# Kernel tuning notes

Measured on AMD Instinct MI355X. Metric: run time of the kernel, lower is better.

## Reference

```python
import jax, jax.numpy as jnp
import numpy as np

N = 20000      # nodes
E = 320000     # edges
F = 32         # node_feat_dim
H = 128        # hidden_dim
HEADS = 4
DH = 128       # out_channels per head (PyG TransformerConv semantics)
L = 2          # number of GNNBlocks actually built


def _ln(x, s, b, eps=1e-5):
    m = x.mean(-1, keepdims=True)
    v = ((x - m) ** 2).mean(-1, keepdims=True)
    return (x - m) / jnp.sqrt(v + eps) * s + b


def setup_inputs() -> dict:
    key = jax.random.key(0)
    ks = jax.random.split(key, 16)
    nrm = lambda k, sh, sc=0.05: jax.random.normal(k, sh, dtype=jnp.float32) * sc
    inp = {}
    inp['x'] = jax.random.normal(ks[0], (N, F), dtype=jnp.float32)
    inp['edge_index'] = jax.random.randint(ks[1], (2, E), 0, N)
    inp['Win'] = nrm(ks[2], (F, H))
    inp['b_in'] = jnp.zeros((H,), jnp.float32)
    inp['ln1_s'] = jnp.ones((L, H), jnp.float32)
    inp['ln1_b'] = jnp.zeros((L, H), jnp.float32)
    inp['Wq'] = nrm(ks[3], (L, H, HEADS * DH))
    inp['bq'] = jnp.zeros((L, HEADS * DH), jnp.float32)
    inp['Wk'] = nrm(ks[4], (L, H, HEADS * DH))
    inp['bk'] = jnp.zeros((L, HEADS * DH), jnp.float32)
    inp['Wv'] = nrm(ks[5], (L, H, HEADS * DH))
    inp['bv'] = jnp.zeros((L, HEADS * DH), jnp.float32)
    inp['Wskip'] = nrm(ks[6], (L, H, H))
    inp['bskip'] = jnp.zeros((L, H), jnp.float32)
    inp['Wbeta'] = nrm(ks[7], (L, 3 * H, 1))
    inp['ln2_s'] = jnp.ones((L, H), jnp.float32)
    inp['ln2_b'] = jnp.zeros((L, H), jnp.float32)
    inp['W1'] = nrm(ks[8], (L, H, 4 * H))
    inp['b1'] = jnp.zeros((L, 4 * H), jnp.float32)
    inp['W2'] = nrm(ks[9], (L, 4 * H, H))
    inp['b2'] = jnp.zeros((L, H), jnp.float32)
    inp['g1'] = jnp.ones((L,), jnp.float32)
    inp['g2'] = jnp.ones((L,), jnp.float32)
    inp['lno_s'] = jnp.ones((H,), jnp.float32)
    inp['lno_b'] = jnp.zeros((H,), jnp.float32)
    return inp


def reference(x, edge_index, Win, b_in, ln1_s, ln1_b, Wq, bq, Wk, bk, Wv, bv,
              Wskip, bskip, Wbeta, ln2_s, ln2_b, W1, b1, W2, b2, g1, g2,
              lno_s, lno_b):
    src, dst = edge_index[0], edge_index[1]  # messages flow src -> dst
    n = x.shape[0]
    scale = 1.0 / np.sqrt(DH).astype(np.float32)
    h = x @ Win + b_in  # [N,H]
    for l in range(L):
        # --- pre-norm TransformerConv (heads=4, concat=False, beta=True) ---
        hn = _ln(h, ln1_s[l], ln1_b[l])
        q = (hn @ Wq[l] + bq[l]).reshape(n, HEADS, DH)
        k = (hn @ Wk[l] + bk[l]).reshape(n, HEADS, DH)
        v = (hn @ Wv[l] + bv[l]).reshape(n, HEADS, DH)
        # per-edge attention logits [E, HEADS]
        alpha = jnp.einsum('ehd,ehd->eh', q[dst], k[src]) * scale
        # segment softmax over incoming edges of each target node
        amax = jax.ops.segment_max(alpha, dst, num_segments=n)  # [N,HEADS]
        num = jnp.exp(alpha - amax[dst])
        den = jax.ops.segment_sum(num, dst, num_segments=n)      # [N,HEADS]
        a = num / den[dst]                                       # [E,HEADS]
        # scatter-aggregate weighted values, then mean over heads (concat=False)
        agg = jax.ops.segment_sum(a[:, :, None] * v[src], dst, num_segments=n)
        out = agg.mean(axis=1)                                   # [N,H]
        # root skip + beta gate
        xr = hn @ Wskip[l] + bskip[l]
        beta = jax.nn.sigmoid(
            jnp.concatenate([out, xr, out - xr], axis=-1) @ Wbeta[l])  # [N,1]
        attn = beta * xr + (1.0 - beta) * out
        h = h + g1[l] * attn
        # --- pre-norm FFN ---
        hn2 = _ln(h, ln2_s[l], ln2_b[l])
        ffn = jax.nn.gelu(hn2 @ W1[l] + b1[l], approximate=False) @ W2[l] + b2[l]
        h = h + g2[l] * ffn
    return _ln(h, lno_s, lno_b)
```

## Files before the change

kernel.cpp:

```cpp
#include <hip/hip_runtime.h>
#include <hip/hip_bf16.h>
#include <math.h>

#define NN 20000
#define NE 320000

typedef unsigned short ushort_t;
typedef unsigned short ushortx8 __attribute__((ext_vector_type(8)));
typedef short s16x8 __attribute__((ext_vector_type(8)));
typedef float f32x4 __attribute__((ext_vector_type(4)));
typedef float f32x2 __attribute__((ext_vector_type(2)));

__device__ __forceinline__ float us2f(unsigned short u){
  return __uint_as_float(((unsigned)u) << 16);
}
__device__ __forceinline__ unsigned short f2us(float f){
  unsigned u = __float_as_uint(f);
  unsigned r = (u + 0x7fffu + ((u >> 16) & 1u)) >> 16;
  return (unsigned short)r;
}
__device__ __forceinline__ void e4m3x8_to_f32(uint2 d, float* out){
  f32x2 a = __builtin_amdgcn_cvt_pk_f32_fp8(d.x, false);
  f32x2 b = __builtin_amdgcn_cvt_pk_f32_fp8(d.x, true);
  f32x2 c = __builtin_amdgcn_cvt_pk_f32_fp8(d.y, false);
  f32x2 e = __builtin_amdgcn_cvt_pk_f32_fp8(d.y, true);
  out[0] = a.x; out[1] = a.y; out[2] = b.x; out[3] = b.y;
  out[4] = c.x; out[5] = c.y; out[6] = e.x; out[7] = e.y;
}
__device__ __forceinline__ uint2 f32x8_to_e4m3(const float* f){
  unsigned lo = __builtin_amdgcn_cvt_pk_fp8_f32(f[0], f[1], 0u, false);
  lo = __builtin_amdgcn_cvt_pk_fp8_f32(f[2], f[3], lo, true);
  unsigned hi = __builtin_amdgcn_cvt_pk_fp8_f32(f[4], f[5], 0u, false);
  hi = __builtin_amdgcn_cvt_pk_fp8_f32(f[6], f[7], hi, true);
  return make_uint2(lo, hi);
}
template<int CTRL>
__device__ __forceinline__ float dpp_add(float x){
  int t = __builtin_amdgcn_update_dpp(0, __float_as_int(x), CTRL, 0xf, 0xf, true);
  return x + __int_as_float(t);
}
__device__ __forceinline__ float red16(float p){
  p = dpp_add<0xB1>(p);
  p = dpp_add<0x4E>(p);
  p = dpp_add<0x141>(p);
  p = dpp_add<0x140>(p);
  return p;
}

__global__ void k_hist(const int* __restrict__ ei, int* __restrict__ deg){
  int e = blockIdx.x * 256 + threadIdx.x;
  if (e < NE) atomicAdd(&deg[ei[NE + e]], 1);
}

__global__ __launch_bounds__(1024) void k_scan(const int* __restrict__ deg,
                                               int* __restrict__ rowst,
                                               int* __restrict__ cur){
  __shared__ int ws[16];
  int tid = threadIdx.x;
  int lane = tid & 63, wid = tid >> 6;
  int base = tid * 20;
  int v[20];
  int s = 0;
  #pragma unroll
  for (int u = 0; u < 20; u++){
    int i = base + u;
    int d = (i < NN) ? deg[i] : 0;
    v[u] = s;
    s += d;
  }
  int incl = s;
  #pragma unroll
  for (int off = 1; off < 64; off <<= 1){
    int t = __shfl_up(incl, off);
    if (lane >= off) incl += t;
  }
  if (lane == 63) ws[wid] = incl;
  __syncthreads();
  int woff = 0;
  #pragma unroll
  for (int k2 = 0; k2 < 16; k2++) if (k2 < wid) woff += ws[k2];
  int toff = woff + incl - s;
  #pragma unroll
  for (int u = 0; u < 20; u++){
    int i = base + u;
    if (i < NN){ int e = toff + v[u]; rowst[i] = e; cur[i] = e; }
  }
  if (tid == 1023) rowst[NN] = toff + s;
}

__global__ void k_scatter(const int* __restrict__ ei, int* __restrict__ cur,
                          int* __restrict__ srcs){
  int e = blockIdx.x * 256 + threadIdx.x;
  if (e < NE){
    int s = ei[e];
    int d = ei[NE + e];
    int p = atomicAdd(&cur[d], 1);
    srcs[p] = s;
  }
}

__global__ void k_wt(const float* __restrict__ Wq, const float* __restrict__ Wk,
                     const float* __restrict__ Wv, const float* __restrict__ Wsk,
                     const float* __restrict__ W1, const float* __restrict__ W2,
                     const float* __restrict__ bq, const float* __restrict__ bk,
                     const float* __restrict__ bv, const float* __restrict__ bsk,
                     ushort_t* __restrict__ out, float* __restrict__ bcat,
                     int* __restrict__ deg){
  int f = blockIdx.x * 256 + threadIdx.x;
  if (f < 688128){
    float val;
    if (f < 425984){
      int l = f / 212992, idx = f % 212992;
      int n = idx / 128, kk = idx % 128;
      if (n < 512)       val = Wq[(size_t)l * 65536 + kk * 512 + n];
      else if (n < 1024) val = Wk[(size_t)l * 65536 + kk * 512 + (n - 512)];
      else if (n < 1536) val = Wv[(size_t)l * 65536 + kk * 512 + (n - 1024)];
      else               val = Wsk[(size_t)l * 16384 + kk * 128 + (n - 1536)];
    } else if (f < 557056){
      int idx = f - 425984;
      int l = idx / 65536, r = idx % 65536;
      int n = r / 128, kk = r % 128;
      val = W1[(size_t)l * 65536 + kk * 512 + n];
    } else {
      int idx = f - 557056;
      int l = idx / 65536, r = idx % 65536;
      int n = r / 512, kk = r % 512;
      val = W2[(size_t)l * 65536 + kk * 128 + n];
    }
    out[f] = f2us(val);
  } else if (f < 691456){
    int i = f - 688128;
    int l = i / 1664, c = i % 1664;
    float v;
    if (c < 512)       v = bq[l * 512 + c];
    else if (c < 1024) v = bk[l * 512 + c - 512];
    else if (c < 1536) v = bv[l * 512 + c - 1024];
    else               v = bsk[l * 128 + c - 1536];
    bcat[i] = v;
  } else if (f < 711456){
    deg[f - 691456] = 0;
  }
}

__global__ __launch_bounds__(128) void k_inproj(const float* __restrict__ x,
                                                const float* __restrict__ Win,
                                                const float* __restrict__ bin,
                                                float* __restrict__ h,
                                                const float* __restrict__ sc,
                                                const float* __restrict__ bi,
                                                ushort_t* __restrict__ hn){
  __shared__ float sW[32 * 128];
  __shared__ float sx[16][32];
  int tid = threadIdx.x;
  for (int i = 0; i < 32; i++) sW[i * 128 + tid] = Win[i * 128 + tid];
  int r0 = blockIdx.x * 16;
  for (int rr = tid >> 5; rr < 16; rr += 4){
    int gr = r0 + rr;
    sx[rr][tid & 31] = (gr < NN) ? x[(size_t)gr * 32 + (tid & 31)] : 0.f;
  }
  __syncthreads();
  float bias = bin[tid];
  for (int r = 0; r < 16; r++){
    int gr = r0 + r;
    if (gr >= NN) break;
    float acc = bias;
    #pragma unroll
    for (int k2 = 0; k2 < 32; k2++) acc += sx[r][k2] * sW[k2 * 128 + tid];
    h[(size_t)gr * 128 + tid] = acc;
  }
  __threadfence_block();
  __syncthreads();
  int lane = tid & 63, wv = tid >> 6;
  for (int rr = 0; rr < 8; rr++){
    int r = wv * 8 + rr;
    int gr = r0 + r;
    if (gr >= NN) continue;
    const float* p = h + (size_t)gr * 128 + lane * 2;
    float x0 = p[0], x1 = p[1];
    float sum = x0 + x1;
    for (int m = 1; m < 64; m <<= 1) sum += __shfl_xor(sum, m);
    float mean = sum * (1.f / 128.f);
    float d0 = x0 - mean, d1 = x1 - mean;
    float vs = d0 * d0 + d1 * d1;
    for (int m = 1; m < 64; m <<= 1) vs += __shfl_xor(vs, m);
    float rstd = rsqrtf(vs * (1.f / 128.f) + 1e-5f);
    int d = lane * 2;
    ushort_t* o = hn + (size_t)gr * 128 + d;
    o[0] = f2us(d0 * rstd * sc[d] + bi[d]);
    o[1] = f2us(d1 * rstd * sc[d + 1] + bi[d + 1]);
  }
}

template<int OUTBF16>
__global__ void k_ln(const float* __restrict__ in, const float* __restrict__ sc,
                     const float* __restrict__ bi, void* __restrict__ outp, int rows){
  int row = blockIdx.x * 4 + (threadIdx.x >> 6);
  int lane = threadIdx.x & 63;
  if (row >= rows) return;
  const float* p = in + (size_t)row * 128 + lane * 2;
  float x0 = p[0], x1 = p[1];
  float sum = x0 + x1;
  for (int m = 1; m < 64; m <<= 1) sum += __shfl_xor(sum, m);
  float mean = sum * (1.f / 128.f);
  float d0 = x0 - mean, d1 = x1 - mean;
  float vs = d0 * d0 + d1 * d1;
  for (int m = 1; m < 64; m <<= 1) vs += __shfl_xor(vs, m);
  float rstd = rsqrtf(vs * (1.f / 128.f) + 1e-5f);
  int d = lane * 2;
  float o0 = d0 * rstd * sc[d] + bi[d];
  float o1 = d1 * rstd * sc[d + 1] + bi[d + 1];
  if (OUTBF16){
    ushort_t* o = (ushort_t*)outp + (size_t)row * 128 + d;
    o[0] = f2us(o0); o[1] = f2us(o1);
  } else {
    float* o = (float*)outp + (size_t)row * 128 + d;
    o[0] = o0; o[1] = o1;
  }
}

template<int MODE>
__global__ __launch_bounds__(256) void k_mm(const ushort_t* __restrict__ A, int M, int K,
                                            const ushort_t* __restrict__ Bt,
                                            const float* __restrict__ bias,
                                            void* __restrict__ Cp, int ldc,
                                            const float* __restrict__ gptr,
                                            ushort_t* __restrict__ qout,
                                            unsigned char* __restrict__ kvout,
                                            ushort_t* __restrict__ xrout,
                                            int nbn){
  __shared__ ushort_t smem[2 * 128 * 72];
  ushort_t* As = smem;
  ushort_t* Bs = smem + 128 * 72;
  int tid = threadIdx.x;
  int nwg = gridDim.x;
  int orig = blockIdx.x;
  int q8 = nwg >> 3, r8 = nwg & 7;
  int xcd = orig & 7, jj = orig >> 3;
  int wgid = (xcd < r8) ? (xcd * (q8 + 1) + jj)
                        : (r8 * (q8 + 1) + (xcd - r8) * q8 + jj);
  int m0 = (wgid / nbn) * 128, n0 = (wgid % nbn) * 128;
  int lane = tid & 63, w = tid >> 6;
  int wm = (w >> 1) * 64, wn = (w & 1) * 64;
  int fr = lane & 15, fq = lane >> 4;
  f32x4 acc[4][4];
  #pragma unroll
  for (int i = 0; i < 4; i++)
    #pragma unroll
    for (int j = 0; j < 4; j++) acc[i][j] = (f32x4){0.f, 0.f, 0.f, 0.f};

  for (int k0 = 0; k0 < K; k0 += 64){
    __syncthreads();
    #pragma unroll
    for (int it = 0; it < 4; it++){
      int idx = it * 256 + tid;
      int row = idx >> 3, ks = (idx & 7) * 8;
      int gr = m0 + row; if (gr >= M) gr = M - 1;
      *(ushortx8*)&As[row * 72 + ks] = *(const ushortx8*)(A + (size_t)gr * K + k0 + ks);
      *(ushortx8*)&Bs[row * 72 + ks] = *(const ushortx8*)(Bt + (size_t)(n0 + row) * K + k0 + ks);
    }
    __syncthreads();
    #pragma unroll
    for (int ks = 0; ks < 64; ks += 32){
      s16x8 a[4], b[4];
      #pragma unroll
      for (int i = 0; i < 4; i++)
        a[i] = *(const s16x8*)&As[(wm + i * 16 + fr) * 72 + ks + fq * 8];
      #pragma unroll
      for (int j = 0; j < 4; j++)
        b[j] = *(const s16x8*)&Bs[(wn + j * 16 + fr) * 72 + ks + fq * 8];
      #pragma unroll
      for (int i = 0; i < 4; i++)
        #pragma unroll
        for (int j = 0; j < 4; j++)
          acc[i][j] = __builtin_amdgcn_mfma_f32_16x16x32_bf16(a[i], b[j], acc[i][j], 0, 0, 0);
    }
  }

  if (MODE == 2){
    float g = *gptr;
    #pragma unroll
    for (int i = 0; i < 4; i++){
      int grb = m0 + wm + i * 16 + fq * 4;
      #pragma unroll
      for (int r = 0; r < 4; r++){
        int gr = grb + r;
        if (gr >= M) continue;
        #pragma unroll
        for (int j = 0; j < 4; j++){
          int gc = n0 + wn + j * 16 + fr;
          float c = acc[i][j][r] + bias[gc];
          ((float*)Cp)[(size_t)gr * ldc + gc] += g * c;
        }
      }
    }
    return;
  }

  __syncthreads();
  ushort_t* Cs = smem;
  #pragma unroll
  for (int i = 0; i < 4; i++){
    int rowb = wm + i * 16 + fq * 4;
    #pragma unroll
    for (int j = 0; j < 4; j++){
      int col = wn + j * 16 + fr;
      float bv = bias[n0 + col];
      #pragma unroll
      for (int r = 0; r < 4; r++){
        float c = acc[i][j][r] + bv;
        if (MODE == 1) c = 0.5f * c * (1.f + erff(c * 0.70710678118654752f));
        Cs[(rowb + r) * 136 + col] = f2us(c);
      }
    }
  }
  __syncthreads();
  #pragma unroll
  for (int it = 0; it < 8; it++){
    int idx = it * 256 + tid;
    int row = idx >> 4, seg = idx & 15;
    int gr = m0 + row;
    if (gr >= M) continue;
    ushortx8 cv = *(const ushortx8*)&Cs[row * 136 + seg * 8];
    int gc = n0 + seg * 8;
    if (MODE == 1){
      *(ushortx8*)((ushort_t*)Cp + (size_t)gr * ldc + gc) = cv;
    } else {
      if (n0 < 512){
        *(ushortx8*)(qout + (size_t)gr * 512 + gc) = cv;
      } else if (n0 < 1536){
        float fv[8];
        #pragma unroll
        for (int t = 0; t < 8; t++) fv[t] = us2f(cv[t]);
        uint2 pk = f32x8_to_e4m3(fv);
        if (n0 < 1024){
          *(uint2*)(kvout + (size_t)gr * 1024 + (size_t)((gc - 512) >> 3) * 16) = pk;
        } else {
          *(uint2*)(kvout + (size_t)gr * 1024 + (size_t)((gc - 1024) >> 3) * 16 + 8) = pk;
        }
      } else {
        *(ushortx8*)(xrout + (size_t)gr * 128 + (gc - 1536)) = cv;
      }
    }
  }
}

#define EDGE_PROC(KVD) {                                                     \
    float kf[8]; e4m3x8_to_f32(make_uint2((KVD).x, (KVD).y), kf);            \
    float p = 0.f;                                                           \
    _Pragma("unroll")                                                        \
    for (int t = 0; t < 8; t++) p += qf[t] * kf[t];                          \
    p = red16(p);                                                            \
    float wgt = __expf(p * scale);                                           \
    float vf[8]; e4m3x8_to_f32(make_uint2((KVD).z, (KVD).w), vf);            \
    l += wgt;                                                                \
    _Pragma("unroll")                                                        \
    for (int t = 0; t < 8; t++) acc[t] += wgt * vf[t];                       \
  }

__global__ void k_attn(const ushort_t* __restrict__ q, const unsigned char* __restrict__ kv8,
                       const int* __restrict__ rowst, const int* __restrict__ srcs,
                       const ushort_t* __restrict__ xr, const float* __restrict__ Wb,
                       const float* __restrict__ g1p, float* __restrict__ h,
                       const float* __restrict__ sc2, const float* __restrict__ bi2,
                       ushort_t* __restrict__ hn){
  int n = blockIdx.x * 4 + (threadIdx.x >> 6);
  int lane = threadIdx.x & 63;
  if (n >= NN) return;
  int s0 = rowst[n], s1 = rowst[n + 1];
  int deg = s1 - s0;
  float qf[8];
  {
    ushortx8 qv = *((const ushortx8*)(q + (size_t)n * 512) + lane);
    #pragma unroll
    for (int t = 0; t < 8; t++) qf[t] = us2f(qv[t]);
  }
  const float scale = 0.08838834764831845f;
  const uint4* kvb = (const uint4*)kv8;
  float l = 0.f;
  float acc[8] = {0.f, 0.f, 0.f, 0.f, 0.f, 0.f, 0.f, 0.f};
  for (int c0 = s0; c0 < s1; c0 += 64){
    int rem = s1 - c0; if (rem > 64) rem = 64;
    int se = (lane < rem) ? srcs[c0 + lane] : 0;
    int j = 0;
    for (; j + 12 <= rem; j += 12){
      uint4 kvd[12];
      #pragma unroll
      for (int u = 0; u < 12; u++){
        int sv = __builtin_amdgcn_readlane(se, j + u);
        kvd[u] = kvb[(size_t)sv * 64 + lane];
      }
      #pragma unroll
      for (int u = 0; u < 12; u++) EDGE_PROC(kvd[u]);
    }
    for (; j + 4 <= rem; j += 4){
      uint4 kvd[4];
      #pragma unroll
      for (int u = 0; u < 4; u++){
        int sv = __builtin_amdgcn_readlane(se, j + u);
        kvd[u] = kvb[(size_t)sv * 64 + lane];
      }
      #pragma unroll
      for (int u = 0; u < 4; u++) EDGE_PROC(kvd[u]);
    }
    for (; j < rem; j++){
      int sv0 = __builtin_amdgcn_readlane(se, j);
      uint4 kvd = kvb[(size_t)sv0 * 64 + lane];
      EDGE_PROC(kvd);
    }
  }
  float inv = deg ? (0.25f / l) : 0.f;
  #pragma unroll
  for (int t = 0; t < 8; t++){
    float r = acc[t] * inv;
    r += __shfl_xor(r, 16); r += __shfl_xor(r, 32);
    acc[t] = r;
  }
  if (lane < 16){
    int d = lane * 8;
    float xv[8];
    {
      ushortx8 xrv = *(const ushortx8*)(xr + (size_t)n * 128 + d);
      #pragma unroll
      for (int t = 0; t < 8; t++) xv[t] = us2f(xrv[t]);
    }
    float pp = 0.f;
    #pragma unroll
    for (int t = 0; t < 8; t++){
      float w0 = Wb[d + t], w1 = Wb[128 + d + t], w2 = Wb[256 + d + t];
      pp += acc[t] * (w0 + w2) + xv[t] * (w1 - w2);
    }
    pp = red16(pp);
    float beta = 1.f / (1.f + __expf(-pp));
    float g = *g1p;
    float* hp = h + (size_t)n * 128 + d;
    float hv[8];
    {
      float4 h0 = *(const float4*)(hp);
      float4 h1 = *(const float4*)(hp + 4);
      hv[0]=h0.x; hv[1]=h0.y; hv[2]=h0.z; hv[3]=h0.w;
      hv[4]=h1.x; hv[5]=h1.y; hv[6]=h1.z; hv[7]=h1.w;
    }
    #pragma unroll
    for (int t = 0; t < 8; t++)
      hv[t] += g * (beta * xv[t] + (1.f - beta) * acc[t]);
    float s = 0.f;
    #pragma unroll
    for (int t = 0; t < 8; t++) s += hv[t];
    s = red16(s);
    float mean = s * (1.f / 128.f);
    float vs = 0.f;
    #pragma unroll
    for (int t = 0; t < 8; t++){ float dd = hv[t] - mean; vs += dd * dd; }
    vs = red16(vs);
    float rstd = rsqrtf(vs * (1.f / 128.f) + 1e-5f);
    *(float4*)(hp) = make_float4(hv[0], hv[1], hv[2], hv[3]);
    *(float4*)(hp + 4) = make_float4(hv[4], hv[5], hv[6], hv[7]);
    ushortx8 hno;
    #pragma unroll
    for (int t = 0; t < 8; t++)
      hno[t] = f2us((hv[t] - mean) * rstd * sc2[d + t] + bi2[d + t]);
    *(ushortx8*)(hn + (size_t)n * 128 + d) = hno;
  }
}

extern "C" void kernel_launch(void* const* d_in, const int* in_sizes, int n_in,
                              void* d_out, int out_size, void* d_ws, size_t ws_size,
                              hipStream_t stream){
  const float* x    = (const float*)d_in[0];
  const int*   ei   = (const int*)d_in[1];
  const float* Win  = (const float*)d_in[2];
  const float* bin  = (const float*)d_in[3];
  const float* ln1s = (const float*)d_in[4];
  const float* ln1b = (const float*)d_in[5];
  const float* Wq   = (const float*)d_in[6];
  const float* bq   = (const float*)d_in[7];
  const float* Wk   = (const float*)d_in[8];
  const float* bk   = (const float*)d_in[9];
  const float* Wv   = (const float*)d_in[10];
  const float* bv   = (const float*)d_in[11];
  const float* Wsk  = (const float*)d_in[12];
  const float* bsk  = (const float*)d_in[13];
  const float* Wbt  = (const float*)d_in[14];
  const float* ln2s = (const float*)d_in[15];
  const float* ln2b = (const float*)d_in[16];
  const float* W1   = (const float*)d_in[17];
  const float* b1   = (const float*)d_in[18];
  const float* W2   = (const float*)d_in[19];
  const float* b2   = (const float*)d_in[20];
  const float* g1   = (const float*)d_in[21];
  const float* g2   = (const float*)d_in[22];
  const float* lnos = (const float*)d_in[23];
  const float* lnob = (const float*)d_in[24];

  char* wsb = (char*)d_ws;
  size_t off = 0;
  float*         h    = (float*)(wsb + off);         off += (size_t)NN * 128 * 4;
  ushort_t*      hn   = (ushort_t*)(wsb + off);      off += (size_t)NN * 128 * 2;
  ushort_t*      qbuf = (ushort_t*)(wsb + off);      off += (size_t)NN * 512 * 2;
  unsigned char* kv8  = (unsigned char*)(wsb + off); off += (size_t)NN * 1024;
  ushort_t*      xrb  = (ushort_t*)(wsb + off);      off += (size_t)NN * 128 * 2;
  ushort_t*      tb   = (ushort_t*)(wsb + off);      off += (size_t)NN * 512 * 2;
  ushort_t*      wt   = (ushort_t*)(wsb + off);      off += (size_t)688128 * 2;
  float*         bcat = (float*)(wsb + off);         off += (size_t)3328 * 4;
  int*           deg   = (int*)(wsb + off);          off += (size_t)NN * 4;
  int*           rowst = (int*)(wsb + off);          off += (size_t)(NN + 4) * 4;
  int*           cur   = (int*)(wsb + off);          off += (size_t)NN * 4;
  int*           srcs  = (int*)(wsb + off);          off += (size_t)NE * 4;
  ushort_t* Wcat = wt;
  ushort_t* W1t  = wt + 425984;
  ushort_t* W2t  = wt + 557056;

  k_wt<<<2780, 256, 0, stream>>>(Wq, Wk, Wv, Wsk, W1, W2, bq, bk, bv, bsk, wt, bcat, deg);
  k_hist<<<(NE + 255) / 256, 256, 0, stream>>>(ei, deg);
  k_scan<<<1, 1024, 0, stream>>>(deg, rowst, cur);
  k_scatter<<<(NE + 255) / 256, 256, 0, stream>>>(ei, cur, srcs);
  k_inproj<<<NN / 16, 128, 0, stream>>>(x, Win, bin, h, ln1s, ln1b, hn);

  for (int l = 0; l < 2; l++){
    if (l == 1)
      k_ln<1><<<(NN + 3) / 4, 256, 0, stream>>>(h, ln1s + 128, ln1b + 128, hn, NN);
    k_mm<3><<<157 * 13, 256, 0, stream>>>(hn, NN, 128, Wcat + (size_t)l * 212992, bcat + l * 1664,
                                          nullptr, 0, nullptr, qbuf, kv8, xrb, 13);
    k_attn<<<(NN + 3) / 4, 256, 0, stream>>>(qbuf, kv8, rowst, srcs, xrb, Wbt + l * 384,
                                             g1 + l, h, ln2s + l * 128, ln2b + l * 128, hn);
    k_mm<1><<<157 * 4, 256, 0, stream>>>(hn, NN, 128, W1t + (size_t)l * 65536, b1 + l * 512,
                                         tb, 512, nullptr, nullptr, nullptr, nullptr, 4);
    k_mm<2><<<157, 256, 0, stream>>>(tb, NN, 512, W2t + (size_t)l * 65536, b2 + l * 128,
                                     h, 128, g2 + l, nullptr, nullptr, nullptr, 1);
  }
  k_ln<0><<<(NN + 3) / 4, 256, 0, stream>>>(h, lnos, lnob, (float*)d_out, NN);
}
```

Measured before the change: 431.0 us.

## Fuse FFN up/down projections into one kernel and retile attention per node

Adds a k_ffn kernel that computes the W1 GEMM, GELU, and W2 GEMM per 128-row tile, keeping the 512-wide intermediate in shared memory in 128-column chunks. This removes the global bf16 intermediate buffer and one kernel launch. The cost is only 157 blocks using about 104KB of LDS each, so occupancy and parallelism are low. Attention now launches one 64-thread block per node and raises the gather unroll from 12 to 16 edges.

```diff
diff --git a/kernel.cpp b/kernel.cpp
--- a/kernel.cpp
+++ b/kernel.cpp
@@ -276,26 +276,6 @@
     }
   }
 
-  if (MODE == 2){
-    float g = *gptr;
-    #pragma unroll
-    for (int i = 0; i < 4; i++){
-      int grb = m0 + wm + i * 16 + fq * 4;
-      #pragma unroll
-      for (int r = 0; r < 4; r++){
-        int gr = grb + r;
-        if (gr >= M) continue;
-        #pragma unroll
-        for (int j = 0; j < 4; j++){
-          int gc = n0 + wn + j * 16 + fr;
-          float c = acc[i][j][r] + bias[gc];
-          ((float*)Cp)[(size_t)gr * ldc + gc] += g * c;
-        }
-      }
-    }
-    return;
-  }
-
   __syncthreads();
   ushort_t* Cs = smem;
   #pragma unroll
@@ -308,7 +288,6 @@
       #pragma unroll
       for (int r = 0; r < 4; r++){
         float c = acc[i][j][r] + bv;
-        if (MODE == 1) c = 0.5f * c * (1.f + erff(c * 0.70710678118654752f));
         Cs[(rowb + r) * 136 + col] = f2us(c);
       }
     }
@@ -322,23 +301,139 @@
     if (gr >= M) continue;
     ushortx8 cv = *(const ushortx8*)&Cs[row * 136 + seg * 8];
     int gc = n0 + seg * 8;
-    if (MODE == 1){
-      *(ushortx8*)((ushort_t*)Cp + (size_t)gr * ldc + gc) = cv;
+    if (n0 < 512){
+      *(ushortx8*)(qout + (size_t)gr * 512 + gc) = cv;
+    } else if (n0 < 1536){
+      float fv[8];
+      #pragma unroll
+      for (int t = 0; t < 8; t++) fv[t] = us2f(cv[t]);
+      uint2 pk = f32x8_to_e4m3(fv);
+      if (n0 < 1024){
+        *(uint2*)(kvout + (size_t)gr * 1024 + (size_t)((gc - 512) >> 3) * 16) = pk;
+      } else {
+        *(uint2*)(kvout + (size_t)gr * 1024 + (size_t)((gc - 1024) >> 3) * 16 + 8) = pk;
+      }
     } else {
-      if (n0 < 512){
-        *(ushortx8*)(qout + (size_t)gr * 512 + gc) = cv;
-      } else if (n0 < 1536){
-        float fv[8];
+      *(ushortx8*)(xrout + (size_t)gr * 128 + (gc - 1536)) = cv;
+    }
+  }
+}
+
+__global__ __launch_bounds__(256) void k_ffn(const ushort_t* __restrict__ hn, int M,
+                                             const ushort_t* __restrict__ W1t,
+                                             const float* __restrict__ b1,
+                                             const ushort_t* __restrict__ W2t,
+                                             const float* __restrict__ b2,
+                                             const float* __restrict__ gptr,
+                                             float* __restrict__ h){
+  extern __shared__ ushort_t smem[];
+  ushort_t* sA = smem;
+  ushort_t* sI = smem + 128 * 136;
+  ushort_t* sB = smem + 2 * 128 * 136;
+  int tid = threadIdx.x;
+  int m0 = blockIdx.x * 128;
+  int lane = tid & 63, w = tid >> 6;
+  int wm = (w >> 1) * 64, wn = (w & 1) * 64;
+  int fr = lane & 15, fq = lane >> 4;
+
+  #pragma unroll
+  for (int it = 0; it < 8; it++){
+    int idx = it * 256 + tid;
+    int row = idx >> 4, seg = (idx & 15) * 8;
+    int gr = m0 + row; if (gr >= M) gr = M - 1;
+    *(ushortx8*)&sA[row * 136 + seg] = *(const ushortx8*)(hn + (size_t)gr * 128 + seg);
+  }
+
+  f32x4 acc2[4][4];
+  #pragma unroll
+  for (int i = 0; i < 4; i++)
+    #pragma unroll
+    for (int j = 0; j < 4; j++) acc2[i][j] = (f32x4){0.f, 0.f, 0.f, 0.f};
+
+  for (int c = 0; c < 4; c++){
+    __syncthreads();
+    #pragma unroll
+    for (int it = 0; it < 8; it++){
+      int idx = it * 256 + tid;
+      int row = idx >> 4, seg = (idx & 15) * 8;
+      *(ushortx8*)&sB[row * 136 + seg] =
+          *(const ushortx8*)(W1t + (size_t)(c * 128 + row) * 128 + seg);
+    }
+    __syncthreads();
+    f32x4 acc1[4][4];
+    #pragma unroll
+    for (int i = 0; i < 4; i++)
+      #pragma unroll
+      for (int j = 0; j < 4; j++) acc1[i][j] = (f32x4){0.f, 0.f, 0.f, 0.f};
+    #pragma unroll
+    for (int kk = 0; kk < 128; kk += 32){
+      s16x8 a[4], b[4];
+      #pragma unroll
+      for (int i = 0; i < 4; i++)
+        a[i] = *(const s16x8*)&sA[(wm + i * 16 + fr) * 136 + kk + fq * 8];
+      #pragma unroll
+      for (int j = 0; j < 4; j++)
+        b[j] = *(const s16x8*)&sB[(wn + j * 16 + fr) * 136 + kk + fq * 8];
+      #pragma unroll
+      for (int i = 0; i < 4; i++)
         #pragma unroll
-        for (int t = 0; t < 8; t++) fv[t] = us2f(cv[t]);
-        uint2 pk = f32x8_to_e4m3(fv);
-        if (n0 < 1024){
-          *(uint2*)(kvout + (size_t)gr * 1024 + (size_t)((gc - 512) >> 3) * 16) = pk;
-        } else {
-          *(uint2*)(kvout + (size_t)gr * 1024 + (size_t)((gc - 1024) >> 3) * 16 + 8) = pk;
+        for (int j = 0; j < 4; j++)
+          acc1[i][j] = __builtin_amdgcn_mfma_f32_16x16x32_bf16(a[i], b[j], acc1[i][j], 0, 0, 0);
+    }
+    __syncthreads();
+    #pragma unroll
+    for (int i = 0; i < 4; i++){
+      int rowb = wm + i * 16 + fq * 4;
+      #pragma unroll
+      for (int j = 0; j < 4; j++){
+        int col = wn + j * 16 + fr;
+        float bv = b1[c * 128 + col];
+        #pragma unroll
+        for (int r = 0; r < 4; r++){
+          float cx = acc1[i][j][r] + bv;
+          cx = 0.5f * cx * (1.f + erff(cx * 0.70710678118654752f));
+          sI[(rowb + r) * 136 + col] = f2us(cx);
         }
-      } else {
-        *(ushortx8*)(xrout + (size_t)gr * 128 + (gc - 1536)) = cv;
+      }
+    }
+    #pragma unroll
+    for (int it = 0; it < 8; it++){
+      int idx = it * 256 + tid;
+      int row = idx >> 4, seg = (idx & 15) * 8;
+      *(ushortx8*)&sB[row * 136 + seg] =
+          *(const ushortx8*)(W2t + (size_t)row * 512 + c * 128 + seg);
+    }
+    __syncthreads();
+    #pragma unroll
+    for (int kk = 0; kk < 128; kk += 32){
+      s16x8 a[4], b[4];
+      #pragma unroll
+      for (int i = 0; i < 4; i++)
+        a[i] = *(const s16x8*)&sI[(wm + i * 16 + fr) * 136 + kk + fq * 8];
+      #pragma unroll
+      for (int j = 0; j < 4; j++)
+        b[j] = *(const s16x8*)&sB[(wn + j * 16 + fr) * 136 + kk + fq * 8];
+      #pragma unroll
+      for (int i = 0; i < 4; i++)
+        #pragma unroll
+        for (int j = 0; j < 4; j++)
+          acc2[i][j] = __builtin_amdgcn_mfma_f32_16x16x32_bf16(a[i], b[j], acc2[i][j], 0, 0, 0);
+    }
+  }
+
+  float g = *gptr;
+  #pragma unroll
+  for (int i = 0; i < 4; i++){
+    int grb = m0 + wm + i * 16 + fq * 4;
+    #pragma unroll
+    for (int r = 0; r < 4; r++){
+      int gr = grb + r;
+      if (gr >= M) continue;
+      #pragma unroll
+      for (int j = 0; j < 4; j++){
+        int gc = wn + j * 16 + fr;
+        float c = acc2[i][j][r] + b2[gc];
+        h[(size_t)gr * 128 + gc] += g * c;
       }
     }
   }
@@ -357,15 +452,15 @@
     for (int t = 0; t < 8; t++) acc[t] += wgt * vf[t];                       \
   }
 
-__global__ void k_attn(const ushort_t* __restrict__ q, const unsigned char* __restrict__ kv8,
+__global__ __launch_bounds__(64) void k_attn(
+                       const ushort_t* __restrict__ q, const unsigned char* __restrict__ kv8,
                        const int* __restrict__ rowst, const int* __restrict__ srcs,
                        const ushort_t* __restrict__ xr, const float* __restrict__ Wb,
                        const float* __restrict__ g1p, float* __restrict__ h,
                        const float* __restrict__ sc2, const float* __restrict__ bi2,
                        ushort_t* __restrict__ hn){
-  int n = blockIdx.x * 4 + (threadIdx.x >> 6);
-  int lane = threadIdx.x & 63;
-  if (n >= NN) return;
+  int n = blockIdx.x;
+  int lane = threadIdx.x;
   int s0 = rowst[n], s1 = rowst[n + 1];
   int deg = s1 - s0;
   float qf[8];
@@ -382,15 +477,15 @@
     int rem = s1 - c0; if (rem > 64) rem = 64;
     int se = (lane < rem) ? srcs[c0 + lane] : 0;
     int j = 0;
-    for (; j + 12 <= rem; j += 12){
-      uint4 kvd[12];
-      #pragma unroll
-      for (int u = 0; u < 12; u++){
+    for (; j + 16 <= rem; j += 16){
+      uint4 kvd[16];
+      #pragma unroll
+      for (int u = 0; u < 16; u++){
         int sv = __builtin_amdgcn_readlane(se, j + u);
         kvd[u] = kvb[(size_t)sv * 64 + lane];
       }
       #pragma unroll
-      for (int u = 0; u < 12; u++) EDGE_PROC(kvd[u]);
+      for (int u = 0; u < 16; u++) EDGE_PROC(kvd[u]);
     }
     for (; j + 4 <= rem; j += 4){
       uint4 kvd[4];
@@ -499,7 +594,6 @@
   ushort_t*      qbuf = (ushort_t*)(wsb + off);      off += (size_t)NN * 512 * 2;
   unsigned char* kv8  = (unsigned char*)(wsb + off); off += (size_t)NN * 1024;
   ushort_t*      xrb  = (ushort_t*)(wsb + off);      off += (size_t)NN * 128 * 2;
-  ushort_t*      tb   = (ushort_t*)(wsb + off);      off += (size_t)NN * 512 * 2;
   ushort_t*      wt   = (ushort_t*)(wsb + off);      off += (size_t)688128 * 2;
   float*         bcat = (float*)(wsb + off);         off += (size_t)3328 * 4;
   int*           deg   = (int*)(wsb + off);          off += (size_t)NN * 4;
@@ -516,17 +610,16 @@
   k_scatter<<<(NE + 255) / 256, 256, 0, stream>>>(ei, cur, srcs);
   k_inproj<<<NN / 16, 128, 0, stream>>>(x, Win, bin, h, ln1s, ln1b, hn);
 
+  const int ffn_lds = 3 * 128 * 136 * 2;
   for (int l = 0; l < 2; l++){
     if (l == 1)
       k_ln<1><<<(NN + 3) / 4, 256, 0, stream>>>(h, ln1s + 128, ln1b + 128, hn, NN);
     k_mm<3><<<157 * 13, 256, 0, stream>>>(hn, NN, 128, Wcat + (size_t)l * 212992, bcat + l * 1664,
                                           nullptr, 0, nullptr, qbuf, kv8, xrb, 13);
-    k_attn<<<(NN + 3) / 4, 256, 0, stream>>>(qbuf, kv8, rowst, srcs, xrb, Wbt + l * 384,
-                                             g1 + l, h, ln2s + l * 128, ln2b + l * 128, hn);
-    k_mm<1><<<157 * 4, 256, 0, stream>>>(hn, NN, 128, W1t + (size_t)l * 65536, b1 + l * 512,
-                                         tb, 512, nullptr, nullptr, nullptr, nullptr, 4);
-    k_mm<2><<<157, 256, 0, stream>>>(tb, NN, 512, W2t + (size_t)l * 65536, b2 + l * 128,
-                                     h, 128, g2 + l, nullptr, nullptr, nullptr, 1);
+    k_attn<<<NN, 64, 0, stream>>>(qbuf, kv8, rowst, srcs, xrb, Wbt + l * 384,
+                                  g1 + l, h, ln2s + l * 128, ln2b + l * 128, hn);
+    k_ffn<<<157, 256, ffn_lds, stream>>>(hn, NN, W1t + (size_t)l * 65536, b1 + l * 512,
+                                         W2t + (size_t)l * 65536, b2 + l * 128, g2 + l, h);
   }
   k_ln<0><<<(NN + 3) / 4, 256, 0, stream>>>(h, lnos, lnob, (float*)d_out, NN);
 }
```

Result: slower. 461.1 us (+7.0%).

## Sort nodes by in-degree so attention blocks get balanced wavefronts

Applied to the files above, without the earlier changes.

Adds a counting sort of nodes by in-degree (histogram, scan, scatter) and has the attention kernel process nodes in that permuted order. Each 4-wave block then handles nodes of similar degree, which reduces divergence in per-wave loop trip counts and idle waves inside a block. The cost is three extra small kernels per call, plus the loss of node locality for the q/xr/h accesses, since nodes within a block are no longer contiguous.

```diff
diff --git a/kernel.cpp b/kernel.cpp
--- a/kernel.cpp
+++ b/kernel.cpp
@@ -96,6 +96,38 @@
     int d = ei[NE + e];
     int p = atomicAdd(&cur[d], 1);
     srcs[p] = s;
+  }
+}
+
+__global__ void k_dhist(const int* __restrict__ deg, int* __restrict__ dcnt){
+  int n = blockIdx.x * 256 + threadIdx.x;
+  if (n < NN){
+    int d = deg[n]; if (d > 127) d = 127;
+    atomicAdd(&dcnt[d], 1);
+  }
+}
+__global__ __launch_bounds__(64) void k_dscan(const int* __restrict__ dcnt,
+                                              int* __restrict__ dcur){
+  int lane = threadIdx.x;
+  int v0 = dcnt[lane * 2], v1 = dcnt[lane * 2 + 1];
+  int s = v0 + v1;
+  int incl = s;
+  #pragma unroll
+  for (int off = 1; off < 64; off <<= 1){
+    int t = __shfl_up(incl, off);
+    if (lane >= off) incl += t;
+  }
+  int excl = incl - s;
+  dcur[lane * 2] = excl;
+  dcur[lane * 2 + 1] = excl + v0;
+}
+__global__ void k_dscatter(const int* __restrict__ deg, int* __restrict__ dcur,
+                           int* __restrict__ perm){
+  int n = blockIdx.x * 256 + threadIdx.x;
+  if (n < NN){
+    int d = deg[n]; if (d > 127) d = 127;
+    int p = atomicAdd(&dcur[d], 1);
+    perm[p] = n;
   }
 }
 
@@ -137,7 +169,7 @@
     else if (c < 1536) v = bv[l * 512 + c - 1024];
     else               v = bsk[l * 128 + c - 1536];
     bcat[i] = v;
-  } else if (f < 711456){
+  } else if (f < 711584){
     deg[f - 691456] = 0;
   }
 }
@@ -357,15 +389,18 @@
     for (int t = 0; t < 8; t++) acc[t] += wgt * vf[t];                       \
   }
 
-__global__ void k_attn(const ushort_t* __restrict__ q, const unsigned char* __restrict__ kv8,
+__global__ __launch_bounds__(256) void k_attn(
+                       const ushort_t* __restrict__ q, const unsigned char* __restrict__ kv8,
                        const int* __restrict__ rowst, const int* __restrict__ srcs,
+                       const int* __restrict__ perm,
                        const ushort_t* __restrict__ xr, const float* __restrict__ Wb,
                        const float* __restrict__ g1p, float* __restrict__ h,
                        const float* __restrict__ sc2, const float* __restrict__ bi2,
                        ushort_t* __restrict__ hn){
-  int n = blockIdx.x * 4 + (threadIdx.x >> 6);
+  int idx = blockIdx.x * 4 + (threadIdx.x >> 6);
   int lane = threadIdx.x & 63;
-  if (n >= NN) return;
+  if (idx >= NN) return;
+  int n = perm[idx];
   int s0 = rowst[n], s1 = rowst[n + 1];
   int deg = s1 - s0;
   float qf[8];
@@ -502,10 +537,13 @@
   ushort_t*      tb   = (ushort_t*)(wsb + off);      off += (size_t)NN * 512 * 2;
   ushort_t*      wt   = (ushort_t*)(wsb + off);      off += (size_t)688128 * 2;
   float*         bcat = (float*)(wsb + off);         off += (size_t)3328 * 4;
-  int*           deg   = (int*)(wsb + off);          off += (size_t)NN * 4;
+  int*           deg   = (int*)(wsb + off);          off += (size_t)(NN + 128) * 4;
   int*           rowst = (int*)(wsb + off);          off += (size_t)(NN + 4) * 4;
   int*           cur   = (int*)(wsb + off);          off += (size_t)NN * 4;
   int*           srcs  = (int*)(wsb + off);          off += (size_t)NE * 4;
+  int*           dcur  = (int*)(wsb + off);          off += (size_t)128 * 4;
+  int*           perm  = (int*)(wsb + off);          off += (size_t)NN * 4;
+  int* dcnt = deg + NN;
   ushort_t* Wcat = wt;
   ushort_t* W1t  = wt + 425984;
   ushort_t* W2t  = wt + 557056;
@@ -514,6 +552,9 @@
   k_hist<<<(NE + 255) / 256, 256, 0, stream>>>(ei, deg);
   k_scan<<<1, 1024, 0, stream>>>(deg, rowst, cur);
   k_scatter<<<(NE + 255) / 256, 256, 0, stream>>>(ei, cur, srcs);
+  k_dhist<<<(NN + 255) / 256, 256, 0, stream>>>(deg, dcnt);
+  k_dscan<<<1, 64, 0, stream>>>(dcnt, dcur);
+  k_dscatter<<<(NN + 255) / 256, 256, 0, stream>>>(deg, dcur, perm);
   k_inproj<<<NN / 16, 128, 0, stream>>>(x, Win, bin, h, ln1s, ln1b, hn);
 
   for (int l = 0; l < 2; l++){
@@ -521,7 +562,7 @@
       k_ln<1><<<(NN + 3) / 4, 256, 0, stream>>>(h, ln1s + 128, ln1b + 128, hn, NN);
     k_mm<3><<<157 * 13, 256, 0, stream>>>(hn, NN, 128, Wcat + (size_t)l * 212992, bcat + l * 1664,
                                           nullptr, 0, nullptr, qbuf, kv8, xrb, 13);
-    k_attn<<<(NN + 3) / 4, 256, 0, stream>>>(qbuf, kv8, rowst, srcs, xrb, Wbt + l * 384,
+    k_attn<<<(NN + 3) / 4, 256, 0, stream>>>(qbuf, kv8, rowst, srcs, perm, xrb, Wbt + l * 384,
                                              g1 + l, h, ln2s + l * 128, ln2b + l * 128, hn);
     k_mm<1><<<157 * 4, 256, 0, stream>>>(hn, NN, 128, W1t + (size_t)l * 65536, b1 + l * 512,
                                          tb, 512, nullptr, nullptr, nullptr, nullptr, 4);
```

Measured after the change: 561.5 us. +30.3%, slower.
